# Kernel optimization log

Hardware: AMD Instinct MI355X
Metric: run time of the kernel (lower is better)

The kernel has to match this reference:

```python
import jax, jax.numpy as jnp
import numpy as np

D_MODEL = 1024
N_HEADS = 16
DEPTH = D_MODEL // N_HEADS  # 64
BATCH, SEQ = 4, 2048


def setup_inputs() -> dict:
    key = jax.random.key(0)
    ks = jax.random.split(key, 8)
    x = jax.random.normal(ks[0], (BATCH, SEQ, D_MODEL), dtype=jnp.float32)
    # Per-head Dense(depth) weights stacked over heads: [H, d_model, depth]
    s = 1.0 / np.sqrt(D_MODEL)
    Wq = jax.random.normal(ks[1], (N_HEADS, D_MODEL, DEPTH), dtype=jnp.float32) * s
    Wk = jax.random.normal(ks[2], (N_HEADS, D_MODEL, DEPTH), dtype=jnp.float32) * s
    Wv = jax.random.normal(ks[3], (N_HEADS, D_MODEL, DEPTH), dtype=jnp.float32) * s
    bq = jnp.zeros((N_HEADS, DEPTH), dtype=jnp.float32)
    bk = jnp.zeros((N_HEADS, DEPTH), dtype=jnp.float32)
    bv = jnp.zeros((N_HEADS, DEPTH), dtype=jnp.float32)
    Wo = jax.random.normal(ks[4], (D_MODEL, D_MODEL), dtype=jnp.float32) * s
    bo = jnp.zeros((D_MODEL,), dtype=jnp.float32)
    return {"x": x, "Wq": Wq, "bq": bq, "Wk": Wk, "bk": bk,
            "Wv": Wv, "bv": bv, "Wo": Wo, "bo": bo}


def reference(x, Wq, bq, Wk, bk, Wv, bv, Wo, bo):
    # Per-head projections, batched over heads: [b, h, s, depth]
    q = jnp.einsum('bsd,hde->bhse', x, Wq) + bq[None, :, None, :]
    k = jnp.einsum('bsd,hde->bhse', x, Wk) + bk[None, :, None, :]
    v = jnp.einsum('bsd,hde->bhse', x, Wv) + bv[None, :, None, :]
    scale = 1.0 / jnp.sqrt(jnp.float32(DEPTH))
    scores = jnp.einsum('bhqe,bhke->bhqk', q, k) * scale  # [b, h, s, s]
    attn = jax.nn.softmax(scores, axis=-1)
    z = jnp.einsum('bhqk,bhke->bhqe', attn, v)  # [b, h, s, depth]
    # Concat heads along last axis (head-major order matches tf.concat of per-head outputs)
    multi_head = z.transpose(0, 2, 1, 3).reshape(BATCH, SEQ, D_MODEL)
    return multi_head @ Wo + bo
```

## Files before the change

### kernel.cpp

```cpp
#include <hip/hip_runtime.h>

typedef unsigned short u16;
typedef __bf16 bf16x8 __attribute__((ext_vector_type(8)));
typedef float f32x4 __attribute__((ext_vector_type(4)));
typedef float f32x16 __attribute__((ext_vector_type(16)));
typedef unsigned int u32x4 __attribute__((ext_vector_type(4)));
typedef unsigned int u32x2 __attribute__((ext_vector_type(2)));

__device__ __forceinline__ u16 f2b(float f) {
  union { float f; unsigned u; } v; v.f = f;
  return (u16)((v.u + 0x7fffu + ((v.u >> 16) & 1u)) >> 16);
}

__device__ __forceinline__ unsigned pkbf(float a, float b) {
#if __has_builtin(__builtin_amdgcn_cvt_pk_bf16_f32)
  typedef __bf16 bf16x2v __attribute__((ext_vector_type(2)));
  bf16x2v r = __builtin_amdgcn_cvt_pk_bf16_f32(a, b);
  return __builtin_bit_cast(unsigned, r);
#else
  unsigned ua = __builtin_bit_cast(unsigned, a) + 0x8000u;
  unsigned ub = __builtin_bit_cast(unsigned, b) + 0x8000u;
  return __builtin_amdgcn_perm(ub, ua, 0x07060302u);
#endif
}

__device__ __forceinline__ float fexp2(float x) {
#if __has_builtin(__builtin_amdgcn_exp2f)
  return __builtin_amdgcn_exp2f(x);
#else
  return exp2f(x);
#endif
}

__device__ __forceinline__ bf16x8 ldfrag(const u16* p) {
  u32x4 r = *(const u32x4*)p;
  return __builtin_bit_cast(bf16x8, r);
}

__device__ __forceinline__ void plswap(unsigned& dst, unsigned& src) {
  asm("v_permlane32_swap_b32 %0, %1" : "+v"(dst), "+v"(src));
}

__device__ __forceinline__ float sum16(const f32x16& v) {
  float a = (v[0] + v[1]) + (v[2] + v[3]);
  float b = (v[4] + v[5]) + (v[6] + v[7]);
  float c = (v[8] + v[9]) + (v[10] + v[11]);
  float d = (v[12] + v[13]) + (v[14] + v[15]);
  return (a + b) + (c + d);
}

__device__ __forceinline__ void build_frags(const f32x16& sc, bf16x8& fLo, bf16x8& fHi) {
  unsigned a0 = pkbf(sc[0], sc[1]);
  unsigned a1 = pkbf(sc[2], sc[3]);
  unsigned b0 = pkbf(sc[4], sc[5]);
  unsigned b1 = pkbf(sc[6], sc[7]);
  plswap(a0, b0);
  plswap(a1, b1);
  u32x4 f; f[0] = a0; f[1] = a1; f[2] = b0; f[3] = b1;
  fLo = __builtin_bit_cast(bf16x8, f);
  unsigned c0 = pkbf(sc[8], sc[9]);
  unsigned c1 = pkbf(sc[10], sc[11]);
  unsigned d0 = pkbf(sc[12], sc[13]);
  unsigned d1 = pkbf(sc[14], sc[15]);
  plswap(c0, d0);
  plswap(c1, d1);
  u32x4 g; g[0] = c0; g[1] = c1; g[2] = d0; g[3] = d1;
  fHi = __builtin_bit_cast(bf16x8, g);
}

#define GLOAD_LDS16(gp, lp)                                                        \
  __builtin_amdgcn_global_load_lds((const __attribute__((address_space(1))) void*)(gp), \
                                   (__attribute__((address_space(3))) void*)(lp), 16, 0, 0)

#define MFMA32(a, b, c) __builtin_amdgcn_mfma_f32_32x32x16_bf16((a), (b), (c), 0, 0, 0)

#define QSC 0.18033688011f


__global__ __launch_bounds__(256) void k_pack(const float* __restrict__ x,
                                              const float* __restrict__ Wq,
                                              const float* __restrict__ Wk,
                                              const float* __restrict__ Wv,
                                              const float* __restrict__ Wo,
                                              u16* __restrict__ xb,
                                              u16* __restrict__ wqkv,
                                              u16* __restrict__ wo_t) {
  const int bid = blockIdx.x, tid = threadIdx.x;
  if (bid < 4096) {
    int i = (bid * 256 + tid) * 8;
    float4 v0 = *(const float4*)(x + i);
    float4 v1 = *(const float4*)(x + i + 4);
    u32x4 o;
    o[0] = pkbf(v0.x, v0.y);
    o[1] = pkbf(v0.z, v0.w);
    o[2] = pkbf(v1.x, v1.y);
    o[3] = pkbf(v1.z, v1.w);
    *(u32x4*)(xb + i) = o;
    return;
  }
  __shared__ u16 tile[64][65];
  if (bid < 4864) {
    int b2 = bid - 4096;
    int p = b2 >> 8, rem = b2 & 255, h = rem >> 4, dt = rem & 15;
    const float* W = (p == 0) ? Wq : (p == 1) ? Wk : Wv;
    for (int i = tid; i < 4096; i += 256) {
      int d = i >> 6, e = i & 63;
      tile[e][d] = f2b(W[h * 65536 + (dt * 64 + d) * 64 + e]);
    }
    __syncthreads();
    for (int i = tid; i < 4096; i += 256) {
      int e = i >> 6, d = i & 63;
      wqkv[(size_t)(p * 1024 + h * 64 + e) * 1024 + dt * 64 + d] = tile[e][d];
    }
  } else {
    int b2 = bid - 4864;
    int kt = b2 >> 4, nt = b2 & 15;
    for (int i = tid; i < 4096; i += 256) {
      int dk = i >> 6, de = i & 63;
      tile[de][dk] = f2b(Wo[(size_t)(kt * 64 + dk) * 1024 + nt * 64 + de]);
    }
    __syncthreads();
    for (int i = tid; i < 4096; i += 256) {
      int de = i >> 6, dk = i & 63;
      wo_t[(size_t)(nt * 64 + de) * 1024 + kt * 64 + dk] = tile[de][dk];
    }
  }
}


template <bool SWAP>
__device__ __forceinline__ void gemm_core32(const u16* __restrict__ A, const u16* __restrict__ Bt,
                                            int row0, int col0, u16* As, u16* Bs, f32x16 acc[2][2]) {
  const int tid = threadIdx.x, w = tid >> 6, lane = tid & 63;
  const int l31 = lane & 31, hi = lane >> 5;
  const int wm = (w >> 1) * 64, wn = (w & 1) * 64;

  int r_[2], c_[2];
#pragma unroll
  for (int i = 0; i < 2; i++) {
    int X = (w * 2 + i) * 1024 + lane * 16;
    int e = (X ^ (((X >> 7) & 7) << 4)) >> 1;
    r_[i] = e >> 5;
    c_[i] = e & 31;
  }
  int oa[2][2], ob[2][2];
#pragma unroll
  for (int t = 0; t < 2; t++)
#pragma unroll
    for (int s = 0; s < 2; s++) {
      int Pa = (wm + t * 32 + l31) * 64 + s * 32 + hi * 16;
      int Pb = (wn + t * 32 + l31) * 64 + s * 32 + hi * 16;
      oa[t][s] = (Pa ^ (((Pa >> 7) & 7) << 4)) >> 1;
      ob[t][s] = (Pb ^ (((Pb >> 7) & 7) << 4)) >> 1;
    }

  const u16* Ag = A + (size_t)row0 * 1024;
  const u16* Bg = Bt + (size_t)col0 * 1024;

#pragma unroll
  for (int i = 0; i < 2; i++) {
    GLOAD_LDS16(Ag + (size_t)r_[i] * 1024 + c_[i], As + (w * 2 + i) * 512);
    GLOAD_LDS16(Bg + (size_t)r_[i] * 1024 + c_[i], Bs + (w * 2 + i) * 512);
  }
  __syncthreads();

  int cur = 0;
  for (int k0 = 0; k0 < 1024; k0 += 32) {
    if (k0 + 32 < 1024) {
      u16* Ad = As + (cur ^ 1) * 4096 + (w * 2) * 512;
      u16* Bd = Bs + (cur ^ 1) * 4096 + (w * 2) * 512;
#pragma unroll
      for (int i = 0; i < 2; i++) {
        GLOAD_LDS16(Ag + (size_t)r_[i] * 1024 + k0 + 32 + c_[i], Ad + i * 512);
        GLOAD_LDS16(Bg + (size_t)r_[i] * 1024 + k0 + 32 + c_[i], Bd + i * 512);
      }
    }
    const u16* Ab = As + cur * 4096;
    const u16* Bb = Bs + cur * 4096;
    bf16x8 af[2][2], bfr[2][2];
#pragma unroll
    for (int t = 0; t < 2; t++)
#pragma unroll
      for (int s = 0; s < 2; s++) {
        af[t][s] = ldfrag(Ab + oa[t][s]);
        bfr[t][s] = ldfrag(Bb + ob[t][s]);
      }
    __builtin_amdgcn_s_setprio(1);
#pragma unroll
    for (int mt = 0; mt < 2; mt++)
#pragma unroll
      for (int nt = 0; nt < 2; nt++)
#pragma unroll
        for (int s = 0; s < 2; s++)
          acc[mt][nt] = SWAP ? MFMA32(bfr[nt][s], af[mt][s], acc[mt][nt])
                             : MFMA32(af[mt][s], bfr[nt][s], acc[mt][nt]);
    __builtin_amdgcn_s_setprio(0);
    __syncthreads();
    cur ^= 1;
  }
}


__global__ __launch_bounds__(256) void k_gemm_qkv(const u16* __restrict__ xb, const u16* __restrict__ wt,
                                                  const float* __restrict__ bq, const float* __restrict__ bk,
                                                  const float* __restrict__ bv,
                                                  u16* __restrict__ qo, u16* __restrict__ ko,
                                                  u16* __restrict__ vto) {
  __shared__ u16 As[8192], Bs[8192];
  f32x16 acc[2][2];
#pragma unroll
  for (int a = 0; a < 2; a++)
#pragma unroll
    for (int b = 0; b < 2; b++)
#pragma unroll
      for (int r = 0; r < 16; r++) acc[a][b][r] = 0.f;

  const int row0 = blockIdx.x * 128, col0 = blockIdx.y * 128;
  const int p = blockIdx.y >> 3;
  const int colr = (blockIdx.y & 7) * 128;
  const int tid = threadIdx.x, w = tid >> 6, lane = tid & 63;
  const int l31 = lane & 31, hi = lane >> 5;
  const int wm = (w >> 1) * 64, wn = (w & 1) * 64;

  if (p == 2) {
    gemm_core32<true>(xb, wt, row0, col0, As, Bs, acc);
#pragma unroll
    for (int mt = 0; mt < 2; mt++) {
      int rb = row0 + wm + mt * 32;
      int b_ = rb >> 11;
      int s_ = (rb & 2047) + l31;
#pragma unroll
      for (int nt = 0; nt < 2; nt++) {
        int ebase = colr + wn + nt * 32;
#pragma unroll
        for (int g = 0; g < 4; g++) {
          float4 bvv = *(const float4*)(bv + ebase + g * 8 + hi * 4);
#pragma unroll
          for (int j = 0; j < 4; j++) {
            int rem = ebase + g * 8 + hi * 4 + j;
            int h = rem >> 6, e = rem & 63;
            float val = acc[mt][nt][g * 4 + j] + (&bvv.x)[j];
            vto[(((size_t)(b_ * 16 + h)) * 64 + e) * 2048 + s_] = f2b(val);
          }
        }
      }
    }
  } else {
    gemm_core32<false>(xb, wt, row0, col0, As, Bs, acc);
    u16* dst = (p == 0) ? qo : ko;
    const float* bias = (p == 0) ? bq : bk;
    const float qsc = (p == 0) ? QSC : 1.0f;
#pragma unroll
    for (int nt = 0; nt < 2; nt++) {
      int rem = colr + wn + nt * 32 + l31;
      int h = rem >> 6, e = rem & 63;
      float bval = bias[rem];
#pragma unroll
      for (int mt = 0; mt < 2; mt++) {
        int rb = row0 + wm + mt * 32;
        int b_ = rb >> 11, sb = rb & 2047;
        size_t obase = ((size_t)(b_ * 16 + h) * 2048) * 64 + e;
#pragma unroll
        for (int reg = 0; reg < 16; reg++) {
          int s_ = sb + (reg & 3) + 8 * (reg >> 2) + 4 * hi;
          float val = (acc[mt][nt][reg] + bval) * qsc;
          dst[obase + (size_t)s_ * 64] = f2b(val);
        }
      }
    }
  }
}


__global__ __launch_bounds__(256) void k_gemm_out(const u16* __restrict__ zb, const u16* __restrict__ wt,
                                                  const float* __restrict__ bo, float* __restrict__ out) {
  __shared__ u16 As[8192], Bs[8192];
  f32x16 acc[2][2];
#pragma unroll
  for (int a = 0; a < 2; a++)
#pragma unroll
    for (int b = 0; b < 2; b++)
#pragma unroll
      for (int r = 0; r < 16; r++) acc[a][b][r] = 0.f;

  const int row0 = blockIdx.x * 128, col0 = blockIdx.y * 128;
  gemm_core32<false>(zb, wt, row0, col0, As, Bs, acc);

  const int tid = threadIdx.x, w = tid >> 6, lane = tid & 63;
  const int l31 = lane & 31, hi = lane >> 5;
  const int wm = (w >> 1) * 64, wn = (w & 1) * 64;
#pragma unroll
  for (int nt = 0; nt < 2; nt++) {
    int c = col0 + wn + nt * 32 + l31;
    float bval = bo[c];
#pragma unroll
    for (int mt = 0; mt < 2; mt++) {
      int rb = row0 + wm + mt * 32;
#pragma unroll
      for (int reg = 0; reg < 16; reg++) {
        int r = rb + (reg & 3) + 8 * (reg >> 2) + 4 * hi;
        out[(size_t)r * 1024 + c] = acc[mt][nt][reg] + bval;
      }
    }
  }
}


__global__ __launch_bounds__(256, 2) void k_attn(const u16* __restrict__ q, const u16* __restrict__ k,
                                                 const u16* __restrict__ vt, u16* __restrict__ z) {
  __shared__ u16 Ks[2][64 * 72], Vs[2][64 * 72];
  const int tid = threadIdx.x, w = tid >> 6, lane = tid & 63;
  const int l31 = lane & 31, hi = lane >> 5;
  const int bh = blockIdx.y, s0 = blockIdx.x * 256;
  const size_t base = (size_t)bh * 2048 * 64;
  const int qrow0 = s0 + w * 64;

  bf16x8 qf[2][4];
#pragma unroll
  for (int u = 0; u < 2; u++) {
    const u16* qp = q + base + (size_t)(qrow0 + u * 32 + l31) * 64 + hi * 8;
#pragma unroll
    for (int ks = 0; ks < 4; ks++) qf[u][ks] = ldfrag(qp + ks * 16);
  }

  f32x16 accT[2][2];
  float ls[2] = {0.f, 0.f};
#pragma unroll
  for (int u = 0; u < 2; u++)
#pragma unroll
    for (int r = 0; r < 16; r++) { accT[u][0][r] = 0.f; accT[u][1][r] = 0.f; }

  const int srow = tid >> 3;
  const int scol = (tid & 7) * 8;
  const u16* kg = k + base;
  const u16* vg = vt + base;

  u32x4 kr0 = *(const u32x4*)(kg + (size_t)srow * 64 + scol);
  u32x4 kr1 = *(const u32x4*)(kg + (size_t)(srow + 32) * 64 + scol);
  u32x4 vr0 = *(const u32x4*)(vg + (size_t)srow * 2048 + scol);
  u32x4 vr1 = *(const u32x4*)(vg + (size_t)(srow + 32) * 2048 + scol);
  *(u32x4*)&Ks[0][srow * 72 + scol] = kr0;
  *(u32x4*)&Ks[0][(srow + 32) * 72 + scol] = kr1;
  *(u32x4*)&Vs[0][srow * 72 + scol] = vr0;
  *(u32x4*)&Vs[0][(srow + 32) * 72 + scol] = vr1;
  kr0 = *(const u32x4*)(kg + (size_t)(64 + srow) * 64 + scol);
  kr1 = *(const u32x4*)(kg + (size_t)(64 + srow + 32) * 64 + scol);
  vr0 = *(const u32x4*)(vg + (size_t)srow * 2048 + 64 + scol);
  vr1 = *(const u32x4*)(vg + (size_t)(srow + 32) * 2048 + 64 + scol);
  __syncthreads();

  for (int kc = 0; kc < 2048; kc += 64) {
    const int buf = (kc >> 6) & 1;
    const u16* Kb = &Ks[buf][0];
    const u16* Vb = &Vs[buf][0];

    bf16x8 pf[2][4];
#pragma unroll
    for (int t = 0; t < 2; t++) {
      f32x16 scA, scB;
#pragma unroll
      for (int r = 0; r < 16; r++) { scA[r] = 0.f; scB[r] = 0.f; }
      __builtin_amdgcn_s_setprio(1);
#pragma unroll
      for (int ks = 0; ks < 4; ks++) {
        bf16x8 kf = ldfrag(Kb + (t * 32 + l31) * 72 + ks * 16 + hi * 8);
        scA = MFMA32(kf, qf[0][ks], scA);
        scB = MFMA32(kf, qf[1][ks], scB);
      }
      __builtin_amdgcn_s_setprio(0);
#pragma unroll
      for (int r = 0; r < 16; r++) scA[r] = fexp2(scA[r]);
#pragma unroll
      for (int r = 0; r < 16; r++) scB[r] = fexp2(scB[r]);
      ls[0] += sum16(scA);
      ls[1] += sum16(scB);
      build_frags(scA, pf[0][2 * t], pf[0][2 * t + 1]);
      build_frags(scB, pf[1][2 * t], pf[1][2 * t + 1]);
    }

    if (kc + 64 < 2048) {
      *(u32x4*)&Ks[buf ^ 1][srow * 72 + scol] = kr0;
      *(u32x4*)&Ks[buf ^ 1][(srow + 32) * 72 + scol] = kr1;
      *(u32x4*)&Vs[buf ^ 1][srow * 72 + scol] = vr0;
      *(u32x4*)&Vs[buf ^ 1][(srow + 32) * 72 + scol] = vr1;
      if (kc + 128 < 2048) {
        int kn = kc + 128;
        kr0 = *(const u32x4*)(kg + (size_t)(kn + srow) * 64 + scol);
        kr1 = *(const u32x4*)(kg + (size_t)(kn + srow + 32) * 64 + scol);
        vr0 = *(const u32x4*)(vg + (size_t)srow * 2048 + kn + scol);
        vr1 = *(const u32x4*)(vg + (size_t)(srow + 32) * 2048 + kn + scol);
      }
    }

    __builtin_amdgcn_s_setprio(1);
#pragma unroll
    for (int ks = 0; ks < 4; ks++) {
      bf16x8 vf0 = ldfrag(Vb + (0 * 32 + l31) * 72 + ks * 16 + hi * 8);
      bf16x8 vf1 = ldfrag(Vb + (1 * 32 + l31) * 72 + ks * 16 + hi * 8);
      accT[0][0] = MFMA32(vf0, pf[0][ks], accT[0][0]);
      accT[0][1] = MFMA32(vf1, pf[0][ks], accT[0][1]);
      accT[1][0] = MFMA32(vf0, pf[1][ks], accT[1][0]);
      accT[1][1] = MFMA32(vf1, pf[1][ks], accT[1][1]);
    }
    __builtin_amdgcn_s_setprio(0);
    __syncthreads();
  }

  const int b_ = bh >> 4, h = bh & 15;
#pragma unroll
  for (int u = 0; u < 2; u++) {
    float l = ls[u];
    l += __shfl_xor(l, 32);
    float inv = 1.f / l;
    int qrow = qrow0 + u * 32 + l31;
    u16* zr = z + ((size_t)(b_ * 2048 + qrow)) * 1024 + h * 64;
#pragma unroll
    for (int et = 0; et < 2; et++)
#pragma unroll
      for (int rr = 0; rr < 16; rr += 2) {
        unsigned pkd = pkbf(accT[u][et][rr] * inv, accT[u][et][rr + 1] * inv);
        int e = et * 32 + (rr & 3) + 8 * (rr >> 2) + 4 * hi;
        *(unsigned*)&zr[e] = pkd;
      }
  }
}


extern "C" void kernel_launch(void* const* d_in, const int* in_sizes, int n_in,
                              void* d_out, int out_size, void* d_ws, size_t ws_size,
                              hipStream_t stream) {
  (void)in_sizes; (void)n_in; (void)out_size;
  const float* x  = (const float*)d_in[0];
  const float* Wq = (const float*)d_in[1];
  const float* bq = (const float*)d_in[2];
  const float* Wk = (const float*)d_in[3];
  const float* bk = (const float*)d_in[4];
  const float* Wv = (const float*)d_in[5];
  const float* bv = (const float*)d_in[6];
  const float* Wo = (const float*)d_in[7];
  const float* bo = (const float*)d_in[8];
  float* out = (float*)d_out;
  char* ws = (char*)d_ws;
  if (ws_size < 92274688u) return;

  u16* xb   = (u16*)(ws + 0);
  u16* wqkv = (u16*)(ws + 16777216);
  u16* wo_t = (u16*)(ws + 23068672);
  u16* qb   = (u16*)(ws + 25165824);
  u16* kb   = (u16*)(ws + 41943040);
  u16* vtb  = (u16*)(ws + 58720256);
  u16* zb   = (u16*)(ws + 75497472);

  k_pack<<<5120, 256, 0, stream>>>(x, Wq, Wk, Wv, Wo, xb, wqkv, wo_t);
  k_gemm_qkv<<<dim3(64, 24), 256, 0, stream>>>(xb, wqkv, bq, bk, bv, qb, kb, vtb);
  k_attn<<<dim3(8, 64), 256, 0, stream>>>(qb, kb, vtb, zb);
  k_gemm_out<<<dim3(64, 8), 256, 0, stream>>>(zb, wo_t, bo, out);
}
```

Baseline: 285.1 us.

## Halve per-warp query rows in attention and raise occupancy hints to four blocks

The attention kernel now gives each warp 32 query rows instead of 64, and each block 128 query rows instead of 256. The grid doubles to 16x64 blocks, and the register footprint per thread (Q fragments, accumulators, P fragments) roughly halves. Launch bounds on attention and both GEMMs ask for 4 blocks per CU to raise occupancy and hide latency. In exchange, each K/V tile loaded into LDS is reused by half as many query rows, so global and LDS traffic for K/V doubles, and the GEMMs may spill under the tighter register cap.

```diff
diff --git a/kernel.cpp b/kernel.cpp
--- a/kernel.cpp
+++ b/kernel.cpp
@@ -201,11 +201,11 @@
 }
 
 
-__global__ __launch_bounds__(256) void k_gemm_qkv(const u16* __restrict__ xb, const u16* __restrict__ wt,
-                                                  const float* __restrict__ bq, const float* __restrict__ bk,
-                                                  const float* __restrict__ bv,
-                                                  u16* __restrict__ qo, u16* __restrict__ ko,
-                                                  u16* __restrict__ vto) {
+__global__ __launch_bounds__(256, 4) void k_gemm_qkv(const u16* __restrict__ xb, const u16* __restrict__ wt,
+                                                     const float* __restrict__ bq, const float* __restrict__ bk,
+                                                     const float* __restrict__ bv,
+                                                     u16* __restrict__ qo, u16* __restrict__ ko,
+                                                     u16* __restrict__ vto) {
   __shared__ u16 As[8192], Bs[8192];
   f32x16 acc[2][2];
 #pragma unroll
@@ -272,8 +272,8 @@
 }
 
 
-__global__ __launch_bounds__(256) void k_gemm_out(const u16* __restrict__ zb, const u16* __restrict__ wt,
-                                                  const float* __restrict__ bo, float* __restrict__ out) {
+__global__ __launch_bounds__(256, 4) void k_gemm_out(const u16* __restrict__ zb, const u16* __restrict__ wt,
+                                                     const float* __restrict__ bo, float* __restrict__ out) {
   __shared__ u16 As[8192], Bs[8192];
   f32x16 acc[2][2];
 #pragma unroll
@@ -306,29 +306,26 @@
 }
 
 
-__global__ __launch_bounds__(256, 2) void k_attn(const u16* __restrict__ q, const u16* __restrict__ k,
+__global__ __launch_bounds__(256, 4) void k_attn(const u16* __restrict__ q, const u16* __restrict__ k,
                                                  const u16* __restrict__ vt, u16* __restrict__ z) {
   __shared__ u16 Ks[2][64 * 72], Vs[2][64 * 72];
   const int tid = threadIdx.x, w = tid >> 6, lane = tid & 63;
   const int l31 = lane & 31, hi = lane >> 5;
-  const int bh = blockIdx.y, s0 = blockIdx.x * 256;
+  const int bh = blockIdx.y, s0 = blockIdx.x * 128;
   const size_t base = (size_t)bh * 2048 * 64;
-  const int qrow0 = s0 + w * 64;
-
-  bf16x8 qf[2][4];
-#pragma unroll
-  for (int u = 0; u < 2; u++) {
-    const u16* qp = q + base + (size_t)(qrow0 + u * 32 + l31) * 64 + hi * 8;
-#pragma unroll
-    for (int ks = 0; ks < 4; ks++) qf[u][ks] = ldfrag(qp + ks * 16);
-  }
-
-  f32x16 accT[2][2];
-  float ls[2] = {0.f, 0.f};
-#pragma unroll
-  for (int u = 0; u < 2; u++)
-#pragma unroll
-    for (int r = 0; r < 16; r++) { accT[u][0][r] = 0.f; accT[u][1][r] = 0.f; }
+  const int qrow0 = s0 + w * 32;
+
+  bf16x8 qf[4];
+  {
+    const u16* qp = q + base + (size_t)(qrow0 + l31) * 64 + hi * 8;
+#pragma unroll
+    for (int ks = 0; ks < 4; ks++) qf[ks] = ldfrag(qp + ks * 16);
+  }
+
+  f32x16 accT[2];
+  float ls = 0.f;
+#pragma unroll
+  for (int r = 0; r < 16; r++) { accT[0][r] = 0.f; accT[1][r] = 0.f; }
 
   const int srow = tid >> 3;
   const int scol = (tid & 7) * 8;
@@ -354,28 +351,23 @@
     const u16* Kb = &Ks[buf][0];
     const u16* Vb = &Vs[buf][0];
 
-    bf16x8 pf[2][4];
+    bf16x8 pf[4];
 #pragma unroll
     for (int t = 0; t < 2; t++) {
-      f32x16 scA, scB;
-#pragma unroll
-      for (int r = 0; r < 16; r++) { scA[r] = 0.f; scB[r] = 0.f; }
+      f32x16 sc;
+#pragma unroll
+      for (int r = 0; r < 16; r++) sc[r] = 0.f;
       __builtin_amdgcn_s_setprio(1);
 #pragma unroll
       for (int ks = 0; ks < 4; ks++) {
         bf16x8 kf = ldfrag(Kb + (t * 32 + l31) * 72 + ks * 16 + hi * 8);
-        scA = MFMA32(kf, qf[0][ks], scA);
-        scB = MFMA32(kf, qf[1][ks], scB);
+        sc = MFMA32(kf, qf[ks], sc);
       }
       __builtin_amdgcn_s_setprio(0);
 #pragma unroll
-      for (int r = 0; r < 16; r++) scA[r] = fexp2(scA[r]);
-#pragma unroll
-      for (int r = 0; r < 16; r++) scB[r] = fexp2(scB[r]);
-      ls[0] += sum16(scA);
-      ls[1] += sum16(scB);
-      build_frags(scA, pf[0][2 * t], pf[0][2 * t + 1]);
-      build_frags(scB, pf[1][2 * t], pf[1][2 * t + 1]);
+      for (int r = 0; r < 16; r++) sc[r] = fexp2(sc[r]);
+      ls += sum16(sc);
+      build_frags(sc, pf[2 * t], pf[2 * t + 1]);
     }
 
     if (kc + 64 < 2048) {
@@ -397,28 +389,25 @@
     for (int ks = 0; ks < 4; ks++) {
       bf16x8 vf0 = ldfrag(Vb + (0 * 32 + l31) * 72 + ks * 16 + hi * 8);
       bf16x8 vf1 = ldfrag(Vb + (1 * 32 + l31) * 72 + ks * 16 + hi * 8);
-      accT[0][0] = MFMA32(vf0, pf[0][ks], accT[0][0]);
-      accT[0][1] = MFMA32(vf1, pf[0][ks], accT[0][1]);
-      accT[1][0] = MFMA32(vf0, pf[1][ks], accT[1][0]);
-      accT[1][1] = MFMA32(vf1, pf[1][ks], accT[1][1]);
+      accT[0] = MFMA32(vf0, pf[ks], accT[0]);
+      accT[1] = MFMA32(vf1, pf[ks], accT[1]);
     }
     __builtin_amdgcn_s_setprio(0);
     __syncthreads();
   }
 
   const int b_ = bh >> 4, h = bh & 15;
-#pragma unroll
-  for (int u = 0; u < 2; u++) {
-    float l = ls[u];
+  {
+    float l = ls;
     l += __shfl_xor(l, 32);
     float inv = 1.f / l;
-    int qrow = qrow0 + u * 32 + l31;
+    int qrow = qrow0 + l31;
     u16* zr = z + ((size_t)(b_ * 2048 + qrow)) * 1024 + h * 64;
 #pragma unroll
     for (int et = 0; et < 2; et++)
 #pragma unroll
       for (int rr = 0; rr < 16; rr += 2) {
-        unsigned pkd = pkbf(accT[u][et][rr] * inv, accT[u][et][rr + 1] * inv);
+        unsigned pkd = pkbf(accT[et][rr] * inv, accT[et][rr + 1] * inv);
         int e = et * 32 + (rr & 3) + 8 * (rr >> 2) + 4 * hi;
         *(unsigned*)&zr[e] = pkd;
       }
@@ -453,6 +442,6 @@
 
   k_pack<<<5120, 256, 0, stream>>>(x, Wq, Wk, Wv, Wo, xb, wqkv, wo_t);
   k_gemm_qkv<<<dim3(64, 24), 256, 0, stream>>>(xb, wqkv, bq, bk, bv, qb, kb, vtb);
-  k_attn<<<dim3(8, 64), 256, 0, stream>>>(qb, kb, vtb, zb);
+  k_attn<<<dim3(16, 64), 256, 0, stream>>>(qb, kb, vtb, zb);
   k_gemm_out<<<dim3(64, 8), 256, 0, stream>>>(zb, wo_t, bo, out);
 }
```

Result: slower. 293.3 us (+2.9%).
